# Optimization experiments

Hardware: AMD Instinct MI355X
Metric: run time of the kernel (lower is better)

## Reference

```python
import jax, jax.numpy as jnp
import numpy as np

D, DFF, H = 768, 3072, 12
HD = D // H
EPS = 1e-12

def _ln(t, gamma, beta):
    mu = t.mean(-1, keepdims=True)
    var = jnp.mean((t - mu) ** 2, -1, keepdims=True)
    return gamma * (t - mu) / jnp.sqrt(var + EPS) + beta

def setup_inputs() -> dict:
    key = jax.random.key(0)
    ks = jax.random.split(key, 16)
    s = 0.02
    x = jax.random.normal(ks[0], (2, 2048, D), jnp.float32)
    mask = jnp.ones((2, 2048), jnp.float32)
    def lin(k, out_d, in_d):
        kw, kb = jax.random.split(k)
        return (jax.random.normal(kw, (out_d, in_d), jnp.float32) * s,
                jnp.zeros((out_d,), jnp.float32))
    Wq, bq = lin(ks[1], D, D)
    Wk, bk = lin(ks[2], D, D)
    Wv, bv = lin(ks[3], D, D)
    Wp, bp = lin(ks[4], D, D)
    W1, bf1 = lin(ks[5], DFF, D)
    W2, bf2 = lin(ks[6], D, DFF)
    g1 = jnp.ones((D,), jnp.float32); be1 = jnp.zeros((D,), jnp.float32)
    g2 = jnp.ones((D,), jnp.float32); be2 = jnp.zeros((D,), jnp.float32)
    return dict(x=x, mask=mask, Wq=Wq, bq=bq, Wk=Wk, bk=bk, Wv=Wv, bv=bv,
                Wp=Wp, bp=bp, g1=g1, be1=be1, W1=W1, bf1=bf1, W2=W2, bf2=bf2,
                g2=g2, be2=be2)

def reference(x, mask, Wq, bq, Wk, bk, Wv, bv, Wp, bp, g1, be1, W1, bf1, W2, bf2, g2, be2):
    B, S, _ = x.shape
    # projections (torch Linear: x @ W^T + b)
    q = (x @ Wq.T + bq).reshape(B, S, H, HD).transpose(0, 2, 1, 3)  # [B,H,S,HD]
    k = (x @ Wk.T + bk).reshape(B, S, H, HD).transpose(0, 2, 1, 3)
    v = (x @ Wv.T + bv).reshape(B, S, H, HD).transpose(0, 2, 1, 3)
    scores = jnp.einsum('bhqd,bhkd->bhqk', q, k) / jnp.sqrt(jnp.float32(HD))
    scores = scores - 10000.0 * (1.0 - mask[:, None, None, :])
    p = jax.nn.softmax(scores, axis=-1)  # dropout is identity at eval
    h = jnp.einsum('bhqk,bhkd->bqhd', p, v).reshape(B, S, D)
    h = h @ Wp.T + bp
    x1 = _ln(x + h, g1, be1)
    ff = jax.nn.gelu(x1 @ W1.T + bf1, approximate=False) @ W2.T + bf2
    return _ln(x1 + ff, g2, be2)
```

## Files before the change

### kernel.cpp

```cpp
#include <hip/hip_runtime.h>
#include <hip/hip_bf16.h>
#include <math.h>

#define D_MODEL 768
#define D_FF    3072
#define N_HEAD  12
#define HEAD_D  64
#define BATCH   2
#define SEQ     2048
#define QKV_LD  2304

typedef __attribute__((ext_vector_type(8))) short short8;
typedef __attribute__((ext_vector_type(8))) unsigned short ushort8;
typedef __attribute__((ext_vector_type(4))) float f32x4;

__device__ inline unsigned short f2bf(float f) {
    union { __hip_bfloat16 b; unsigned short u; } cv;
    cv.b = __float2bfloat16(f);
    return cv.u;
}

__device__ inline float bf2f(unsigned short u) {
    union { unsigned int i; float f; } cv;
    cv.i = ((unsigned int)u) << 16;
    return cv.f;
}

__device__ inline void async_load16(const void* g, void* l) {
    __builtin_amdgcn_global_load_lds(
        (const __attribute__((address_space(1))) void*)g,
        (__attribute__((address_space(3))) void*)l, 16, 0, 0);
}

__global__ __launch_bounds__(256) void conv_fused(
    const float* __restrict__ x,
    const float* __restrict__ Wq, const float* __restrict__ Wk,
    const float* __restrict__ Wv, const float* __restrict__ Wp,
    const float* __restrict__ W1, const float* __restrict__ W2,
    const float* __restrict__ bq, const float* __restrict__ bk,
    const float* __restrict__ bv,
    unsigned short* __restrict__ xb, unsigned short* __restrict__ wqkvb,
    unsigned short* __restrict__ wpb, unsigned short* __restrict__ w1b,
    unsigned short* __restrict__ w2b, float* __restrict__ bqkv)
{
    int bid = blockIdx.x;
    const float* src; unsigned short* dst; int base;
    if      (bid < 3072) { src = x;  dst = xb;              base = bid;        }
    else if (bid < 3648) { src = Wq; dst = wqkvb;           base = bid - 3072; }
    else if (bid < 4224) { src = Wk; dst = wqkvb + 589824;  base = bid - 3648; }
    else if (bid < 4800) { src = Wv; dst = wqkvb + 1179648; base = bid - 4224; }
    else if (bid < 5376) { src = Wp; dst = wpb;             base = bid - 4800; }
    else if (bid < 7680) { src = W1; dst = w1b;             base = bid - 5376; }
    else if (bid < 9984) { src = W2; dst = w2b;             base = bid - 7680; }
    else {
        for (int j = threadIdx.x; j < QKV_LD; j += 256)
            bqkv[j] = (j < 768) ? bq[j] : (j < 1536) ? bk[j - 768] : bv[j - 1536];
        return;
    }
    int i = (base * 256 + threadIdx.x) * 4;
    float4 v = *(const float4*)(src + i);
    ushort4 o4;
    o4.x = f2bf(v.x); o4.y = f2bf(v.y); o4.z = f2bf(v.z); o4.w = f2bf(v.w);
    *(ushort4*)(dst + i) = o4;
}

#define NSTAGE 3

__global__ __launch_bounds__(256) void gemm_bf16(
    const unsigned short* __restrict__ A, int lda,
    const unsigned short* __restrict__ W, int ldw,
    const float* __restrict__ bias,
    const unsigned short* __restrict__ resb, int ldr,
    float* __restrict__ outf, unsigned short* __restrict__ outb,
    float* __restrict__ pacc, int ldo,
    int M, int N, int K, int mode)
{
    __shared__ unsigned short As[NSTAGE][128 * 32];
    __shared__ unsigned short Bs[NSTAGE][128 * 32];

    const int t    = threadIdx.x;
    const int lane = t & 63;
    const int wv   = t >> 6;
    const int wm   = wv >> 1;
    const int wn   = wv & 1;
    const int bm   = blockIdx.y * 128;
    const int bn   = blockIdx.x * 128;
    const int kz   = blockIdx.z;
    const int Kc   = K / gridDim.z;

    const int qd   = lane >> 4;
    const int l16  = lane & 15;

    f32x4 acc[4][4];
    #pragma unroll
    for (int i = 0; i < 4; i++)
        #pragma unroll
        for (int j = 0; j < 4; j++)
            acc[i][j] = (f32x4){0.f, 0.f, 0.f, 0.f};

    const int srow = lane >> 2;
    const int sseg = (lane & 3) * 8;
    const int r0   = (wv * 2 + 0) * 16 + srow;
    const int r1   = (wv * 2 + 1) * 16 + srow;
    const size_t gA0 = (size_t)(bm + r0) * lda + sseg;
    const size_t gA1 = (size_t)(bm + r1) * lda + sseg;
    const size_t gB0 = (size_t)(bn + r0) * ldw + sseg;
    const size_t gB1 = (size_t)(bn + r1) * ldw + sseg;
    const int c0 = (wv * 2 + 0) * 512;
    const int c1 = (wv * 2 + 1) * 512;

    const int kbeg  = kz * Kc;
    const int niter = Kc / 32;

    async_load16(A + gA0 + kbeg, &As[0][c0]);
    async_load16(W + gB0 + kbeg, &Bs[0][c0]);
    async_load16(A + gA1 + kbeg, &As[0][c1]);
    async_load16(W + gB1 + kbeg, &Bs[0][c1]);
    if (niter > 1) {
        async_load16(A + gA0 + kbeg + 32, &As[1][c0]);
        async_load16(W + gB0 + kbeg + 32, &Bs[1][c0]);
        async_load16(A + gA1 + kbeg + 32, &As[1][c1]);
        async_load16(W + gB1 + kbeg + 32, &Bs[1][c1]);
    }

    int stage = 0;
    for (int it = 0; it < niter; it++) {
        if (it + 1 < niter) __builtin_amdgcn_s_waitcnt(0x0F74);
        else                __builtin_amdgcn_s_waitcnt(0x0F70);
        __builtin_amdgcn_s_barrier();

        if (it + 2 < niter) {
            const int sn = (stage + 2 >= NSTAGE) ? stage + 2 - NSTAGE : stage + 2;
            const int kn = kbeg + (it + 2) * 32;
            async_load16(A + gA0 + kn, &As[sn][c0]);
            async_load16(W + gB0 + kn, &Bs[sn][c0]);
            async_load16(A + gA1 + kn, &As[sn][c1]);
            async_load16(W + gB1 + kn, &Bs[sn][c1]);
        }

        short8 af[4], bf[4];
        #pragma unroll
        for (int mt = 0; mt < 4; mt++)
            af[mt] = *(const short8*)(&As[stage][(wm * 64 + mt * 16 + l16) * 32 + qd * 8]);
        #pragma unroll
        for (int nt = 0; nt < 4; nt++)
            bf[nt] = *(const short8*)(&Bs[stage][(wn * 64 + nt * 16 + l16) * 32 + qd * 8]);
        #pragma unroll
        for (int mt = 0; mt < 4; mt++)
            #pragma unroll
            for (int nt = 0; nt < 4; nt++)
                acc[mt][nt] = __builtin_amdgcn_mfma_f32_16x16x32_bf16(
                    af[mt], bf[nt], acc[mt][nt], 0, 0, 0);

        stage = (stage == NSTAGE - 1) ? 0 : stage + 1;
    }

    #pragma unroll
    for (int mt = 0; mt < 4; mt++) {
        #pragma unroll
        for (int nt = 0; nt < 4; nt++) {
            int col = bn + wn * 64 + nt * 16 + l16;
            float bv = (kz == 0) ? bias[col] : 0.f;
            #pragma unroll
            for (int r = 0; r < 4; r++) {
                int row = bm + wm * 64 + mt * 16 + qd * 4 + r;
                if (kz != 0) {
                    pacc[(size_t)row * ldo + col] = acc[mt][nt][r];
                    continue;
                }
                float v = acc[mt][nt][r] + bv;
                if (mode == 1) {
                    v += bf2f(resb[(size_t)row * ldr + col]);
                    outf[(size_t)row * ldo + col] = v;
                } else if (mode == 2) {
                    v = 0.5f * v * (1.0f + erff(v * 0.70710678118654752f));
                    outb[(size_t)row * ldo + col] = f2bf(v);
                } else if (mode == 3) {
                    outb[(size_t)row * ldo + col] = f2bf(v);
                } else {
                    outf[(size_t)row * ldo + col] = v;
                }
            }
        }
    }
}

__global__ __launch_bounds__(256) void vtrans(
    const unsigned short* __restrict__ qkv, unsigned short* __restrict__ vT)
{
    __shared__ unsigned short T[64 * 72];
    const int t   = threadIdx.x;
    const int kt  = blockIdx.x;
    const int bh  = blockIdx.y;
    const int h   = bh % N_HEAD;
    const int b   = bh / N_HEAD;
    const int row = t >> 2;
    const int c0  = (t & 3) * 16;

    const unsigned short* src =
        qkv + (size_t)(b * SEQ + kt * 64 + row) * QKV_LD + 1536 + h * HEAD_D + c0;
    *(ushort8*)&T[row * 72 + c0]     = *(const ushort8*)src;
    *(ushort8*)&T[row * 72 + c0 + 8] = *(const ushort8*)(src + 8);
    __syncthreads();

    const int d = t >> 2;
    ushort8 o0, o1;
    #pragma unroll
    for (int j = 0; j < 8; j++) o0[j] = T[(c0 + j) * 72 + d];
    #pragma unroll
    for (int j = 0; j < 8; j++) o1[j] = T[(c0 + 8 + j) * 72 + d];
    unsigned short* dst = vT + ((size_t)bh * HEAD_D + d) * SEQ + kt * 64 + c0;
    *(ushort8*)dst       = o0;
    *(ushort8*)(dst + 8) = o1;
}

#define ASTR 72

__global__ __launch_bounds__(256) void attn_mfma(
    const unsigned short* __restrict__ qkv, const unsigned short* __restrict__ vT,
    const float* __restrict__ mask, unsigned short* __restrict__ out)
{
    __shared__ __align__(16) unsigned short Ks[64 * ASTR];
    __shared__ __align__(16) unsigned short Vt[64 * ASTR];
    __shared__ float Ms[64];

    const int t    = threadIdx.x;
    const int lane = t & 63;
    const int wv   = t >> 6;
    const int l16  = lane & 15;
    const int quad = lane >> 4;
    const int q0   = blockIdx.x * 64;
    const int bh   = blockIdx.y;
    const int h    = bh % N_HEAD;
    const int b    = bh / N_HEAD;

    const unsigned short* qb  = qkv + (size_t)b * SEQ * QKV_LD + h * HEAD_D;
    const unsigned short* kb  = qb + 768;
    const unsigned short* vtb = vT + (size_t)bh * HEAD_D * SEQ;

    const int srow = t >> 2;
    const int sc0  = (t & 3) * 16;
    const int sigrow = (srow & 0x23) | ((srow & 0x04) << 2) | ((srow & 0x18) >> 1);

    {
        const ushort8* src = (const ushort8*)(qb + (size_t)(q0 + srow) * QKV_LD + sc0);
        *(ushort8*)&Ks[srow * ASTR + sc0]     = src[0];
        *(ushort8*)&Ks[srow * ASTR + sc0 + 8] = src[1];
    }
    __syncthreads();
    short8 bq0 = *(const short8*)&Ks[(wv * 16 + l16) * ASTR + quad * 8];
    short8 bq1 = *(const short8*)&Ks[(wv * 16 + l16) * ASTR + 32 + quad * 8];
    __syncthreads();

    f32x4 o[4];
    #pragma unroll
    for (int i = 0; i < 4; i++) o[i] = (f32x4){0.f, 0.f, 0.f, 0.f};
    float m_st = -INFINITY, l_st = 0.f;

    ushort8 rk0, rk1, rv0, rv1;
    float rm = 1.0f;
    {
        const ushort8* ksrc = (const ushort8*)(kb + (size_t)srow * QKV_LD + sc0);
        rk0 = ksrc[0]; rk1 = ksrc[1];
        const ushort8* vsrc = (const ushort8*)(vtb + (size_t)srow * SEQ + sc0);
        rv0 = vsrc[0]; rv1 = vsrc[1];
        if (t < 64) rm = mask[b * SEQ + t];
    }

    for (int kt = 0; kt < SEQ / 64; kt++) {
        *(ushort8*)&Ks[sigrow * ASTR + sc0]     = rk0;
        *(ushort8*)&Ks[sigrow * ASTR + sc0 + 8] = rk1;
        *(ushort8*)&Vt[srow * ASTR + sc0]       = rv0;
        *(ushort8*)&Vt[srow * ASTR + sc0 + 8]   = rv1;
        if (t < 64) Ms[t] = -10000.0f * (1.0f - rm);
        __syncthreads();

        if (kt + 1 < SEQ / 64) {
            const int kn = (kt + 1) * 64;
            const ushort8* ksrc = (const ushort8*)(kb + (size_t)(kn + srow) * QKV_LD + sc0);
            rk0 = ksrc[0]; rk1 = ksrc[1];
            const ushort8* vsrc = (const ushort8*)(vtb + (size_t)srow * SEQ + kn + sc0);
            rv0 = vsrc[0]; rv1 = vsrc[1];
            if (t < 64) rm = mask[b * SEQ + kn + t];
        }

        f32x4 st[4];
        #pragma unroll
        for (int bi = 0; bi < 4; bi++) {
            const int krow = (bi * 16 + l16) * ASTR;
            short8 k0 = *(const short8*)&Ks[krow + quad * 8];
            short8 k1 = *(const short8*)&Ks[krow + 32 + quad * 8];
            f32x4 z = (f32x4){0.f, 0.f, 0.f, 0.f};
            z = __builtin_amdgcn_mfma_f32_16x16x32_bf16(k0, bq0, z, 0, 0, 0);
            st[bi] = __builtin_amdgcn_mfma_f32_16x16x32_bf16(k1, bq1, z, 0, 0, 0);
        }

        float p[4][4];
        float mx = -3.0e38f;
        #pragma unroll
        for (int bi = 0; bi < 4; bi++) {
            #pragma unroll
            for (int r = 0; r < 4; r++) {
                float s = fmaf(st[bi][r], 0.125f,
                               Ms[((bi >> 1) << 5) + (quad << 3) + ((bi & 1) << 2) + r]);
                p[bi][r] = s;
                mx = fmaxf(mx, s);
            }
        }
        mx = fmaxf(mx, __shfl_xor(mx, 16, 64));
        mx = fmaxf(mx, __shfl_xor(mx, 32, 64));
        float m_new = fmaxf(m_st, mx);
        float alpha = __expf(m_st - m_new);
        m_st = m_new;
        float ls = 0.f;
        #pragma unroll
        for (int bi = 0; bi < 4; bi++) {
            #pragma unroll
            for (int r = 0; r < 4; r++) {
                p[bi][r] = __expf(p[bi][r] - m_new);
                ls += p[bi][r];
            }
        }
        ls += __shfl_xor(ls, 16, 64);
        ls += __shfl_xor(ls, 32, 64);
        l_st = l_st * alpha + ls;

        float ar[4];
        #pragma unroll
        for (int r = 0; r < 4; r++) ar[r] = __shfl(alpha, quad * 4 + r, 64);
        #pragma unroll
        for (int nt = 0; nt < 4; nt++)
            #pragma unroll
            for (int r = 0; r < 4; r++)
                o[nt][r] *= ar[r];

        short8 pf0, pf1;
        #pragma unroll
        for (int bsel = 0; bsel < 2; bsel++) {
            #pragma unroll
            for (int r = 0; r < 4; r++) {
                pf0[bsel * 4 + r] = (short)f2bf(p[bsel][r]);
                pf1[bsel * 4 + r] = (short)f2bf(p[2 + bsel][r]);
            }
        }

        #pragma unroll
        for (int nt = 0; nt < 4; nt++) {
            const int vrow = (nt * 16 + l16) * ASTR;
            short8 v0 = *(const short8*)&Vt[vrow + quad * 8];
            short8 v1 = *(const short8*)&Vt[vrow + 32 + quad * 8];
            o[nt] = __builtin_amdgcn_mfma_f32_16x16x32_bf16(pf0, v0, o[nt], 0, 0, 0);
            o[nt] = __builtin_amdgcn_mfma_f32_16x16x32_bf16(pf1, v1, o[nt], 0, 0, 0);
        }
        __syncthreads();
    }

    float inv = 1.0f / l_st;
    float ir[4];
    #pragma unroll
    for (int r = 0; r < 4; r++) ir[r] = __shfl(inv, quad * 4 + r, 64);
    #pragma unroll
    for (int nt = 0; nt < 4; nt++) {
        #pragma unroll
        for (int r = 0; r < 4; r++) {
            int qi = q0 + wv * 16 + quad * 4 + r;
            out[(size_t)(b * SEQ + qi) * D_MODEL + h * HEAD_D + nt * 16 + l16] =
                f2bf(o[nt][r] * ir[r]);
        }
    }
}

__global__ __launch_bounds__(256) void ln_kernel(
    const float* __restrict__ in, const float* __restrict__ in2,
    const float* __restrict__ g, const float* __restrict__ be,
    float* __restrict__ outf, unsigned short* __restrict__ outb)
{
    const int row = blockIdx.x;
    const int t   = threadIdx.x;
    const float* rp  = in  + (size_t)row * D_MODEL;
    const float* rp2 = in2 ? in2 + (size_t)row * D_MODEL : nullptr;

    float vals[3];
    float s = 0.f, s2 = 0.f;
    #pragma unroll
    for (int i = 0; i < 3; i++) {
        float x = rp[t + i * 256];
        if (rp2) x += rp2[t + i * 256];
        vals[i] = x;
        s += x; s2 += x * x;
    }
    #pragma unroll
    for (int off = 32; off >= 1; off >>= 1) {
        s  += __shfl_xor(s,  off, 64);
        s2 += __shfl_xor(s2, off, 64);
    }
    __shared__ float rs[4], rs2[4];
    __shared__ float mu_s, rstd_s;
    const int wave = t >> 6, lane = t & 63;
    if (lane == 0) { rs[wave] = s; rs2[wave] = s2; }
    __syncthreads();
    if (t == 0) {
        float S1 = rs[0] + rs[1] + rs[2] + rs[3];
        float S2 = rs2[0] + rs2[1] + rs2[2] + rs2[3];
        float mu  = S1 * (1.0f / D_MODEL);
        float var = S2 * (1.0f / D_MODEL) - mu * mu;
        mu_s = mu;
        rstd_s = rsqrtf(var + 1e-12f);
    }
    __syncthreads();
    const float mu = mu_s, rstd = rstd_s;
    #pragma unroll
    for (int i = 0; i < 3; i++) {
        int c = t + i * 256;
        float o = g[c] * (vals[i] - mu) * rstd + be[c];
        if (outf) outf[(size_t)row * D_MODEL + c] = o;
        if (outb) outb[(size_t)row * D_MODEL + c] = f2bf(o);
    }
}

extern "C" void kernel_launch(void* const* d_in, const int* in_sizes, int n_in,
                              void* d_out, int out_size, void* d_ws, size_t ws_size,
                              hipStream_t stream)
{
    const float* x    = (const float*)d_in[0];
    const float* mask = (const float*)d_in[1];
    const float* Wq   = (const float*)d_in[2];
    const float* bq   = (const float*)d_in[3];
    const float* Wk   = (const float*)d_in[4];
    const float* bk   = (const float*)d_in[5];
    const float* Wv   = (const float*)d_in[6];
    const float* bv   = (const float*)d_in[7];
    const float* Wp   = (const float*)d_in[8];
    const float* bp   = (const float*)d_in[9];
    const float* g1   = (const float*)d_in[10];
    const float* be1  = (const float*)d_in[11];
    const float* W1   = (const float*)d_in[12];
    const float* bf1  = (const float*)d_in[13];
    const float* W2   = (const float*)d_in[14];
    const float* bf2  = (const float*)d_in[15];
    const float* g2   = (const float*)d_in[16];
    const float* be2  = (const float*)d_in[17];

    const int M = BATCH * SEQ;

    char* ws = (char*)d_ws;
    unsigned short* qkvb  = (unsigned short*)(ws + 0);
    unsigned short* ff1b  = (unsigned short*)(ws + 0);
    unsigned short* xb    = (unsigned short*)(ws + 25165824);
    unsigned short* hb    = (unsigned short*)(ws + 31457280);
    unsigned short* x1b   = (unsigned short*)(ws + 31457280);
    float*          y0    = (float*)(ws + 37748736);
    unsigned short* wqkvb = (unsigned short*)(ws + 50331648);
    unsigned short* wpb   = (unsigned short*)(ws + 53870592);
    unsigned short* w1b   = (unsigned short*)(ws + 55050240);
    unsigned short* w2b   = (unsigned short*)(ws + 59768832);
    float*          bqkv  = (float*)(ws + 64487424);
    float*          p1    = (float*)(ws + 64496640);
    unsigned short* vTb   = (unsigned short*)(ws + 77079552);

    dim3 blk(256);

    conv_fused<<<dim3(9985), blk, 0, stream>>>(
        x, Wq, Wk, Wv, Wp, W1, W2, bq, bk, bv,
        xb, wqkvb, wpb, w1b, w2b, bqkv);

    gemm_bf16<<<dim3(QKV_LD / 128, M / 128, 1), blk, 0, stream>>>(
        xb, D_MODEL, wqkvb, D_MODEL, bqkv, nullptr, 0,
        nullptr, qkvb, nullptr, QKV_LD, M, QKV_LD, D_MODEL, 3);

    vtrans<<<dim3(SEQ / 64, BATCH * N_HEAD), blk, 0, stream>>>(qkvb, vTb);

    attn_mfma<<<dim3(SEQ / 64, BATCH * N_HEAD), blk, 0, stream>>>(qkvb, vTb, mask, hb);

    gemm_bf16<<<dim3(D_MODEL / 128, M / 128, 2), blk, 0, stream>>>(
        hb, D_MODEL, wpb, D_MODEL, bp, xb, D_MODEL,
        y0, nullptr, p1, D_MODEL, M, D_MODEL, D_MODEL, 1);

    ln_kernel<<<dim3(M), blk, 0, stream>>>(y0, p1, g1, be1, nullptr, x1b);

    gemm_bf16<<<dim3(D_FF / 128, M / 128, 1), blk, 0, stream>>>(
        x1b, D_MODEL, w1b, D_MODEL, bf1, nullptr, 0,
        nullptr, ff1b, nullptr, D_FF, M, D_FF, D_MODEL, 2);

    gemm_bf16<<<dim3(D_MODEL / 128, M / 128, 2), blk, 0, stream>>>(
        ff1b, D_FF, w2b, D_FF, bf2, x1b, D_MODEL,
        y0, nullptr, p1, D_MODEL, M, D_MODEL, D_FF, 1);

    ln_kernel<<<dim3(M), blk, 0, stream>>>(y0, p1, g2, be2, (float*)d_out, nullptr);
}
```

Before: 368.3 us.

## Add dedicated QKV GEMM with 4-stage async pipeline and XCD-aware tile swizzle

Replaces the generic GEMM launch for the QKV projection with a specialized kernel. It uses a four-buffer shared-memory ring with async global-to-LDS loads issued three stages ahead, and waits on explicit counters before each barrier. Block indices are remapped so neighbouring tiles land on the same XCD to improve L2 reuse. This costs more LDS per block (64KB), which may reduce occupancy, and the kernel is hardcoded to the QKV shapes.

```diff
diff --git a/kernel.cpp b/kernel.cpp
--- a/kernel.cpp
+++ b/kernel.cpp
@@ -185,6 +185,114 @@
     }
 }
 
+__global__ __launch_bounds__(256) void gemm_qkv(
+    const unsigned short* __restrict__ A,
+    const unsigned short* __restrict__ W,
+    const float* __restrict__ bias,
+    unsigned short* __restrict__ outb)
+{
+    __shared__ unsigned short As[4][128 * 32];
+    __shared__ unsigned short Bs[4][128 * 32];
+
+    const int t    = threadIdx.x;
+    const int lane = t & 63;
+    const int wv   = t >> 6;
+    const int wm   = wv >> 1;
+    const int wn   = wv & 1;
+
+    const int flat = blockIdx.y * 18 + blockIdx.x;
+    const int xcd  = flat & 7;
+    const int u    = flat >> 3;
+    const int mi   = (xcd >> 1) * 8 + u / 9;
+    const int ni   = (xcd & 1) * 9 + u % 9;
+    const int bm   = mi * 128;
+    const int bn   = ni * 128;
+
+    const int qd   = lane >> 4;
+    const int l16  = lane & 15;
+
+    f32x4 acc[4][4];
+    #pragma unroll
+    for (int i = 0; i < 4; i++)
+        #pragma unroll
+        for (int j = 0; j < 4; j++)
+            acc[i][j] = (f32x4){0.f, 0.f, 0.f, 0.f};
+
+    const int srow = lane >> 2;
+    const int sseg = (lane & 3) * 8;
+    const int r0   = (wv * 2 + 0) * 16 + srow;
+    const int r1   = (wv * 2 + 1) * 16 + srow;
+    const size_t gA0 = (size_t)(bm + r0) * D_MODEL + sseg;
+    const size_t gA1 = (size_t)(bm + r1) * D_MODEL + sseg;
+    const size_t gB0 = (size_t)(bn + r0) * D_MODEL + sseg;
+    const size_t gB1 = (size_t)(bn + r1) * D_MODEL + sseg;
+    const int c0 = (wv * 2 + 0) * 512;
+    const int c1 = (wv * 2 + 1) * 512;
+
+    const int niter = D_MODEL / 32;
+
+    async_load16(A + gA0, &As[0][c0]);
+    async_load16(W + gB0, &Bs[0][c0]);
+    async_load16(A + gA1, &As[0][c1]);
+    async_load16(W + gB1, &Bs[0][c1]);
+    async_load16(A + gA0 + 32, &As[1][c0]);
+    async_load16(W + gB0 + 32, &Bs[1][c0]);
+    async_load16(A + gA1 + 32, &As[1][c1]);
+    async_load16(W + gB1 + 32, &Bs[1][c1]);
+    async_load16(A + gA0 + 64, &As[2][c0]);
+    async_load16(W + gB0 + 64, &Bs[2][c0]);
+    async_load16(A + gA1 + 64, &As[2][c1]);
+    async_load16(W + gB1 + 64, &Bs[2][c1]);
+
+    int stage = 0;
+    for (int it = 0; it < niter; it++) {
+        if      (it + 2 < niter) __builtin_amdgcn_s_waitcnt(0x0F78);
+        else if (it + 1 < niter) __builtin_amdgcn_s_waitcnt(0x0F74);
+        else                     __builtin_amdgcn_s_waitcnt(0x0F70);
+        __builtin_amdgcn_s_barrier();
+
+        if (it + 3 < niter) {
+            int sn = stage + 3;
+            if (sn >= 4) sn -= 4;
+            const int kn = (it + 3) * 32;
+            async_load16(A + gA0 + kn, &As[sn][c0]);
+            async_load16(W + gB0 + kn, &Bs[sn][c0]);
+            async_load16(A + gA1 + kn, &As[sn][c1]);
+            async_load16(W + gB1 + kn, &Bs[sn][c1]);
+        }
+
+        short8 af[4], bf[4];
+        #pragma unroll
+        for (int mt = 0; mt < 4; mt++)
+            af[mt] = *(const short8*)(&As[stage][(wm * 64 + mt * 16 + l16) * 32 + qd * 8]);
+        #pragma unroll
+        for (int nt = 0; nt < 4; nt++)
+            bf[nt] = *(const short8*)(&Bs[stage][(wn * 64 + nt * 16 + l16) * 32 + qd * 8]);
+        #pragma unroll
+        for (int mt = 0; mt < 4; mt++)
+            #pragma unroll
+            for (int nt = 0; nt < 4; nt++)
+                acc[mt][nt] = __builtin_amdgcn_mfma_f32_16x16x32_bf16(
+                    af[mt], bf[nt], acc[mt][nt], 0, 0, 0);
+
+        stage = (stage == 3) ? 0 : stage + 1;
+    }
+
+    #pragma unroll
+    for (int mt = 0; mt < 4; mt++) {
+        #pragma unroll
+        for (int nt = 0; nt < 4; nt++) {
+            int col = bn + wn * 64 + nt * 16 + l16;
+            float bv = bias[col];
+            #pragma unroll
+            for (int r = 0; r < 4; r++) {
+                int row = bm + wm * 64 + mt * 16 + qd * 4 + r;
+                outb[(size_t)row * QKV_LD + col] = f2bf(acc[mt][nt][r] + bv);
+            }
+        }
+    }
+}
+
 __global__ __launch_bounds__(256) void vtrans(
     const unsigned short* __restrict__ qkv, unsigned short* __restrict__ vT)
 {
@@ -464,9 +572,7 @@
         x, Wq, Wk, Wv, Wp, W1, W2, bq, bk, bv,
         xb, wqkvb, wpb, w1b, w2b, bqkv);
 
-    gemm_bf16<<<dim3(QKV_LD / 128, M / 128, 1), blk, 0, stream>>>(
-        xb, D_MODEL, wqkvb, D_MODEL, bqkv, nullptr, 0,
-        nullptr, qkvb, nullptr, QKV_LD, M, QKV_LD, D_MODEL, 3);
+    gemm_qkv<<<dim3(QKV_LD / 128, M / 128), blk, 0, stream>>>(xb, wqkvb, bqkv, qkvb);
 
     vtrans<<<dim3(SEQ / 64, BATCH * N_HEAD), blk, 0, stream>>>(qkvb, vTb);
 
```

After: 362.0 us. About the same (-1.7%).
